# Performance work log

Measured on AMD Instinct MI355X. Metric: run time of the kernel, lower is better.

## Reference

```python
import jax, jax.numpy as jnp
import numpy as np


def _apply_rope(x, cos, sin):
    # x: (b, h, L, D); cos/sin: (b, 1, L, D//2)
    b, h, L, D = x.shape
    xr = x.reshape(b, h, L, D // 2, 2)
    xre, xim = xr[..., 0], xr[..., 1]
    out_re = xre * cos - xim * sin
    out_im = xre * sin + xim * cos
    return jnp.stack([out_re, out_im], axis=-1).reshape(b, h, L, D)


def setup_inputs() -> dict:
    key = jax.random.key(0)
    k1, k2, k3, k4 = jax.random.split(key, 4)
    B, H, L, D = 1, 24, 4096, 128
    q = jax.random.normal(k1, (B, H, L, D), dtype=jnp.float32)
    k = jax.random.normal(k2, (B, H, L, D), dtype=jnp.float32)
    v = jax.random.normal(k3, (B, H, L, D), dtype=jnp.float32)
    positional_encoding = jax.random.normal(k4, (B, L, D // 2, 2), dtype=jnp.float32)
    return {"q": q, "k": k, "v": v, "positional_encoding": positional_encoding}


def reference(q, k, v, positional_encoding):
    # freqs_cis expanded over head axis: (b, 1, L, D//2)
    cos = positional_encoding[:, None, :, :, 0]
    sin = positional_encoding[:, None, :, :, 1]
    qr = _apply_rope(q, cos, sin)
    kr = _apply_rope(k, cos, sin)
    D = q.shape[-1]
    scale = 1.0 / jnp.sqrt(jnp.asarray(D, dtype=q.dtype))
    # (b, h, L, S)
    attn = jnp.einsum("bhld,bhsd->bhls", qr, kr) * scale
    attn = jax.nn.softmax(attn, axis=-1)
    x = jnp.einsum("bhls,bhsd->bhld", attn, v)
    # (b, L, h, d) -> (b, L, h*d)
    b, h, L, d = x.shape
    return jnp.transpose(x, (0, 2, 1, 3)).reshape(b, L, h * d)
```

## Files before the change

kernel.cpp:

```cpp
#include <hip/hip_runtime.h>
#include <hip/hip_bf16.h>

#define H 24
#define L 4096
#define Dh 128
#define QBLK 128
#define KVBLK 64
#define NQT (L/QBLK)
#define NKT (L/KVBLK)

typedef __bf16 bf16;
typedef bf16 bf16x8 __attribute__((ext_vector_type(8)));
typedef bf16 bf16x4 __attribute__((ext_vector_type(4)));
typedef bf16 bf16x2 __attribute__((ext_vector_type(2)));
typedef float f32x4 __attribute__((ext_vector_type(4)));
typedef float f32x16 __attribute__((ext_vector_type(16)));
typedef unsigned u32x4 __attribute__((ext_vector_type(4)));

__device__ __forceinline__ void rope4(const float4& x, const float4& cs, float* o) {
  o[0] = x.x*cs.x - x.y*cs.y;
  o[1] = x.x*cs.y + x.y*cs.x;
  o[2] = x.z*cs.z - x.w*cs.w;
  o[3] = x.z*cs.w + x.w*cs.z;
}

__device__ __forceinline__ unsigned cvt_pk_bf16(float lo, float hi_) {
  unsigned r;
  asm("v_cvt_pk_bf16_f32 %0, %1, %2" : "=v"(r) : "v"(lo), "v"(hi_));
  return r;
}

__device__ __forceinline__ void pl_swap(unsigned &a, unsigned &b) {
#if __has_builtin(__builtin_amdgcn_permlane32_swap)
  typedef unsigned u32x2_t __attribute__((ext_vector_type(2)));
  u32x2_t r = __builtin_amdgcn_permlane32_swap(a, b, false, false);
  a = r.x; b = r.y;
#else
  asm("v_permlane32_swap_b32 %0, %1" : "+v"(a), "+v"(b));
#endif
}

template<int BASE>
__device__ __forceinline__ bf16x8 pack_frag(const f32x16& s) {
  unsigned a0 = cvt_pk_bf16(s[BASE+0], s[BASE+1]);
  unsigned a1 = cvt_pk_bf16(s[BASE+2], s[BASE+3]);
  unsigned b0 = cvt_pk_bf16(s[BASE+4], s[BASE+5]);
  unsigned b1 = cvt_pk_bf16(s[BASE+6], s[BASE+7]);
  pl_swap(a0, b0);
  pl_swap(a1, b1);
  u32x4 v; v[0] = a0; v[1] = a1; v[2] = b0; v[3] = b1;
  return __builtin_bit_cast(bf16x8, v);
}

__device__ __forceinline__ f32x16 zero16() {
  f32x16 v;
#pragma unroll
  for (int i = 0; i < 16; i++) v[i] = 0.f;
  return v;
}

__device__ __forceinline__ void gl16(const void* g, void* l) {
  __builtin_amdgcn_global_load_lds(
      (const __attribute__((address_space(1))) void*)g,
      (__attribute__((address_space(3))) void*)l, 16, 0, 0);
}

__global__ __launch_bounds__(256) void kprep(const float* __restrict__ k,
    const float* __restrict__ pe, bf16* __restrict__ wk) {
  int b = blockIdx.x;
  int h = b >> 7;
  int t = threadIdx.x;
  int l = t & 63, wq = t >> 6, hi = l >> 5;
  int row = (b & 127) * 32 + (l & 31);
  const float* kr = k + ((size_t)h * L + row) * Dh;
  const float* pr = pe + (size_t)row * Dh;
#pragma unroll
  for (int i = 0; i < 2; i++) {
    int ks = wq * 2 + i;
    int d = ks * 16 + hi * 8;
    float4 a  = *(const float4*)(kr + d);
    float4 c  = *(const float4*)(pr + d);
    float4 a2 = *(const float4*)(kr + d + 4);
    float4 c2 = *(const float4*)(pr + d + 4);
    float o[8]; rope4(a, c, o); rope4(a2, c2, o + 4);
    bf16x8 r;
#pragma unroll
    for (int j = 0; j < 8; j++) r[j] = (bf16)o[j];
    *(bf16x8*)(wk + ((size_t)b * 8 + ks) * 512 + l * 8) = r;
  }
}

__global__ __launch_bounds__(256) void vprep(const float* __restrict__ v,
    bf16* __restrict__ wv) {
  __shared__ bf16 T[64][132];
  int b = blockIdx.x;
  int h = b >> 6, G = b & 63;
  int t = threadIdx.x;
  {
    int row = t >> 2, c0 = (t & 3) * 32;
    const float* src = v + ((size_t)h * L + G * 64 + row) * Dh + c0;
#pragma unroll
    for (int i = 0; i < 8; i++) {
      float4 a = ((const float4*)src)[i];
      T[row][c0 + i*4 + 0] = (bf16)a.x; T[row][c0 + i*4 + 1] = (bf16)a.y;
      T[row][c0 + i*4 + 2] = (bf16)a.z; T[row][c0 + i*4 + 3] = (bf16)a.w;
    }
  }
  __syncthreads();
  int l = t & 63, wq = t >> 6, hi = l >> 5, l31 = l & 31;
#pragma unroll
  for (int dt = 0; dt < 4; dt++) {
    bf16x8 r;
#pragma unroll
    for (int j = 0; j < 8; j++) r[j] = T[wq * 16 + hi * 8 + j][dt * 32 + l31];
    *(bf16x8*)(wv + (((size_t)h * 256 + G * 4 + wq) * 4 + dt) * 512 + l * 8) = r;
  }
}

__device__ __forceinline__ void attn5_iter(
    const char* kb, char* kn, int t,
    const char* kg0, const bf16* vgl, int wo, int lane, int hi,
    const bf16x8 (&qf)[8], f32x16 (&acc)[4], float& m, float& lsum) {
  asm volatile("s_waitcnt vmcnt(0)" ::: "memory");
  __builtin_amdgcn_s_barrier();
  __builtin_amdgcn_sched_barrier(0);
  if (t + 1 < NKT) {
    const char* ks_ = kg0 + (size_t)(t + 1) * 16384;
    gl16(ks_,        kn + wo);
    gl16(ks_ + 1024, kn + wo + 1024);
    gl16(ks_ + 2048, kn + wo + 2048);
    gl16(ks_ + 3072, kn + wo + 3072);
  }
  __builtin_amdgcn_sched_barrier(0);

  f32x16 s0 = zero16(), s1 = zero16();
  __builtin_amdgcn_s_setprio(1);
#pragma unroll
  for (int ks = 0; ks < 8; ks++) {
    bf16x8 k0 = *(const bf16x8*)(kb + ks * 1024 + lane * 16);
    s0 = __builtin_amdgcn_mfma_f32_32x32x16_bf16(k0, qf[ks], s0, 0, 0, 0);
    bf16x8 k1 = *(const bf16x8*)(kb + 8192 + ks * 1024 + lane * 16);
    s1 = __builtin_amdgcn_mfma_f32_32x32x16_bf16(k1, qf[ks], s1, 0, 0, 0);
  }
  __builtin_amdgcn_s_setprio(0);

  float t8[8];
#pragma unroll
  for (int i = 0; i < 8; i++)
    t8[i] = fmaxf(fmaxf(s0[i], s0[i + 8]), fmaxf(s1[i], s1[i + 8]));
#pragma unroll
  for (int i = 0; i < 4; i++) t8[i] = fmaxf(t8[i], t8[i + 4]);
  float tm = fmaxf(fmaxf(t8[0], t8[1]), fmaxf(t8[2], t8[3]));
  tm = fmaxf(tm, __shfl_xor(tm, 32, 64));
  if (__any(tm > m + 8.f)) {
    float mn = fmaxf(m, tm);
    float alpha = __builtin_amdgcn_exp2f(m - mn);
    m = mn;
    lsum *= alpha;
#pragma unroll
    for (int r = 0; r < 16; r++) {
      int cr = (r & 3) + 8 * (r >> 2) + 4 * hi;
      float ar = __shfl(alpha, cr, 64);
#pragma unroll
      for (int dt = 0; dt < 4; dt++) acc[dt][r] *= ar;
    }
  }
#pragma unroll
  for (int r = 0; r < 16; r++) {
    s0[r] = __builtin_amdgcn_exp2f(s0[r] - m);
    s1[r] = __builtin_amdgcn_exp2f(s1[r] - m);
  }
  {
    float s8[8];
#pragma unroll
    for (int i = 0; i < 8; i++) s8[i] = (s0[i] + s0[i + 8]) + (s1[i] + s1[i + 8]);
#pragma unroll
    for (int i = 0; i < 4; i++) s8[i] += s8[i + 4];
    float rs = (s8[0] + s8[1]) + (s8[2] + s8[3]);
    rs += __shfl_xor(rs, 32, 64);
    lsum += rs;
  }

  bf16x8 pa00 = pack_frag<0>(s0);
  bf16x8 pa01 = pack_frag<8>(s0);
  bf16x8 pa10 = pack_frag<0>(s1);
  bf16x8 pa11 = pack_frag<8>(s1);

  const bf16* vt = vgl + (size_t)t * 8192;
  __builtin_amdgcn_s_setprio(1);
#pragma unroll
  for (int dt = 0; dt < 4; dt++) {
    bf16x8 v0 = *(const bf16x8*)(vt + (0 * 4 + dt) * 512);
    acc[dt] = __builtin_amdgcn_mfma_f32_32x32x16_bf16(pa00, v0, acc[dt], 0, 0, 0);
    bf16x8 v1 = *(const bf16x8*)(vt + (1 * 4 + dt) * 512);
    acc[dt] = __builtin_amdgcn_mfma_f32_32x32x16_bf16(pa01, v1, acc[dt], 0, 0, 0);
    bf16x8 v2 = *(const bf16x8*)(vt + (2 * 4 + dt) * 512);
    acc[dt] = __builtin_amdgcn_mfma_f32_32x32x16_bf16(pa10, v2, acc[dt], 0, 0, 0);
    bf16x8 v3 = *(const bf16x8*)(vt + (3 * 4 + dt) * 512);
    acc[dt] = __builtin_amdgcn_mfma_f32_32x32x16_bf16(pa11, v3, acc[dt], 0, 0, 0);
  }
  __builtin_amdgcn_s_setprio(0);
}

__global__ __launch_bounds__(256, 3) void attn5(
    const float* __restrict__ q, const float* __restrict__ pe,
    const bf16* __restrict__ wk, const bf16* __restrict__ wv,
    float* __restrict__ out) {
  __shared__ __align__(16) char Kb0[16384], Kb1[16384];

  int bid = (int)blockIdx.x;
  int swz = (bid & 7) * (H * NQT / 8) + (bid >> 3);
  int h = swz >> 5, qt = swz & 31;
  int tid = threadIdx.x;
  int w = tid >> 6, lane = tid & 63;
  int l31 = lane & 31, hi = lane >> 5;
  int wo = w * 4096;

  const float SC = 0.08838834764831845f * 1.4426950408889634f;

  int qrow = qt * QBLK + w * 32 + l31;
  bf16x8 qf[8];
  {
    const float* qp = q + ((size_t)h * L + qrow) * Dh;
    const float* pp = pe + (size_t)qrow * Dh;
#pragma unroll
    for (int ks = 0; ks < 8; ks++) {
      int d = ks * 16 + hi * 8;
      float4 a  = *(const float4*)(qp + d);
      float4 c  = *(const float4*)(pp + d);
      float4 a2 = *(const float4*)(qp + d + 4);
      float4 c2 = *(const float4*)(pp + d + 4);
      float o[8]; rope4(a, c, o); rope4(a2, c2, o + 4);
#pragma unroll
      for (int j = 0; j < 8; j++) qf[ks][j] = (bf16)(o[j] * SC);
    }
  }

  f32x16 acc[4];
#pragma unroll
  for (int dt = 0; dt < 4; dt++) acc[dt] = zero16();
  float m = -3.0e38f, lsum = 0.f;

  const char* kg0 = (const char*)(wk + (size_t)h * 524288) + wo + lane * 16;
  const bf16* vgl = wv + (size_t)h * 524288 + lane * 8;

  gl16(kg0,        Kb0 + wo);
  gl16(kg0 + 1024, Kb0 + wo + 1024);
  gl16(kg0 + 2048, Kb0 + wo + 2048);
  gl16(kg0 + 3072, Kb0 + wo + 3072);

#pragma unroll 1
  for (int tt = 0; tt < NKT / 2; ++tt) {
    attn5_iter(Kb0, Kb1, 2 * tt,     kg0, vgl, wo, lane, hi, qf, acc, m, lsum);
    attn5_iter(Kb1, Kb0, 2 * tt + 1, kg0, vgl, wo, lane, hi, qf, acc, m, lsum);
  }

#pragma unroll
  for (int r = 0; r < 16; r++) {
    int cr = (r & 3) + 8 * (r >> 2) + 4 * hi;
    float ls = __shfl(lsum, cr, 64);
    float inv = 1.0f / ls;
    size_t orow = (size_t)(qt * QBLK + w * 32 + cr);
    float* op = out + orow * (H * Dh) + h * Dh + l31;
#pragma unroll
    for (int dt = 0; dt < 4; dt++) op[dt * 32] = acc[dt][r] * inv;
  }
}

__global__ __launch_bounds__(512) void attn_fb(
    const float* __restrict__ q, const float* __restrict__ kg,
    const float* __restrict__ vg, const float* __restrict__ pe,
    float* __restrict__ out) {
  __shared__ __align__(16) char KsB[KVBLK * Dh * 2];
  __shared__ __align__(16) char VtB[Dh * (KVBLK + 8) * 2];
  __shared__ __align__(16) bf16 Ps[8][16 * KVBLK];

  int bid = (int)blockIdx.x;
  int swz = (bid & 7) * (NQT * H / 8) + (bid >> 3);
  int h  = swz >> 5;
  int qt = swz & 31;
  int tid = threadIdx.x;
  int w = tid >> 6, lane = tid & 63;
  int l16 = lane & 15, lg = lane >> 4;

  const float SC = 0.08838834764831845f * 1.4426950408889634f;

  int qr = qt * QBLK + w * 16 + l16;
  bf16x8 qf[4];
  {
    const float* qrow  = q  + ((size_t)h * L + qr) * Dh;
    const float* perow = pe + (size_t)qr * Dh;
#pragma unroll
    for (int kk = 0; kk < 4; kk++) {
      int d = kk * 32 + lg * 8;
      float4 a  = *(const float4*)(qrow + d);
      float4 b  = *(const float4*)(qrow + d + 4);
      float4 ca = *(const float4*)(perow + d);
      float4 cb = *(const float4*)(perow + d + 4);
      float o[8]; rope4(a, ca, o); rope4(b, cb, o + 4);
#pragma unroll
      for (int j = 0; j < 8; j++) qf[kk][j] = (bf16)(o[j] * SC);
    }
  }

  float m[4], lsum[4];
  f32x4 acc[8];
#pragma unroll
  for (int r = 0; r < 4; r++) { m[r] = -3.0e38f; lsum[r] = 0.f; }
#pragma unroll
  for (int j = 0; j < 8; j++) acc[j] = (f32x4){0.f, 0.f, 0.f, 0.f};

  int krow_s = tid >> 3;
  int kd_s   = (tid & 7) * 16;
  int vd_s   = (tid & 31) * 4;
  int vp_s   = tid >> 5;
  char* psb = (char*)&Ps[w][0];

  for (int t = 0; t < NKT; t++) {
    int kv0 = t * KVBLK;
    {
      bf16 ko[16];
      const float* src = kg + ((size_t)h * L + kv0 + krow_s) * Dh + kd_s;
      const float* ps  = pe + (size_t)(kv0 + krow_s) * Dh + kd_s;
#pragma unroll
      for (int c = 0; c < 4; c++) {
        float4 a  = *(const float4*)(src + c * 4);
        float4 cs = *(const float4*)(ps + c * 4);
        float o[4]; rope4(a, cs, o);
        ko[c*4+0]=(bf16)o[0]; ko[c*4+1]=(bf16)o[1];
        ko[c*4+2]=(bf16)o[2]; ko[c*4+3]=(bf16)o[3];
      }
#pragma unroll
      for (int c = 0; c < 2; c++) {
        int byte = (krow_s * 256 + (kd_s + c * 8) * 2) ^ ((krow_s & 7) << 4);
        *(bf16x8*)(KsB + byte) = *(bf16x8*)(ko + c * 8);
      }
    }
#pragma unroll
    for (int pi = 0; pi < 2; pi++) {
      int p = vp_s + pi * 16;
      int r0 = 2 * p;
      float4 fa = *(const float4*)(vg + ((size_t)h * L + kv0 + r0)     * Dh + vd_s);
      float4 fb = *(const float4*)(vg + ((size_t)h * L + kv0 + r0 + 1) * Dh + vd_s);
      bf16x4 a4, b4;
      a4[0]=(bf16)fa.x; a4[1]=(bf16)fa.y; a4[2]=(bf16)fa.z; a4[3]=(bf16)fa.w;
      b4[0]=(bf16)fb.x; b4[1]=(bf16)fb.y; b4[2]=(bf16)fb.z; b4[3]=(bf16)fb.w;
#pragma unroll
      for (int j = 0; j < 4; j++) {
        bf16x2 pr; pr[0] = a4[j]; pr[1] = b4[j];
        *(bf16x2*)(VtB + (vd_s + j) * 144 + r0 * 2) = pr;
      }
    }
    __syncthreads();

    f32x4 s[4];
#pragma unroll
    for (int jt = 0; jt < 4; jt++) {
      f32x4 a_s = (f32x4){0.f, 0.f, 0.f, 0.f};
      int krow = jt * 16 + l16;
#pragma unroll
      for (int kk = 0; kk < 4; kk++) {
        int byte = (krow * 256 + kk * 64 + lg * 16) ^ ((krow & 7) << 4);
        bf16x8 kf = *(const bf16x8*)(KsB + byte);
        a_s = __builtin_amdgcn_mfma_f32_16x16x32_bf16(qf[kk], kf, a_s, 0, 0, 0);
      }
      s[jt] = a_s;
    }

#pragma unroll
    for (int r = 0; r < 4; r++) {
      float tm = fmaxf(fmaxf(s[0][r], s[1][r]), fmaxf(s[2][r], s[3][r]));
#pragma unroll
      for (int off = 1; off < 16; off <<= 1) tm = fmaxf(tm, __shfl_xor(tm, off, 64));
      float mn = fmaxf(m[r], tm);
      float alpha = exp2f(m[r] - mn);
      m[r] = mn;
      float rs = 0.f;
#pragma unroll
      for (int jt = 0; jt < 4; jt++) {
        float pv_ = exp2f(s[jt][r] - mn);
        s[jt][r] = pv_;
        rs += pv_;
      }
#pragma unroll
      for (int off = 1; off < 16; off <<= 1) rs += __shfl_xor(rs, off, 64);
      lsum[r] = lsum[r] * alpha + rs;
#pragma unroll
      for (int j = 0; j < 8; j++) acc[j][r] *= alpha;
    }

#pragma unroll
    for (int jt = 0; jt < 4; jt++)
#pragma unroll
      for (int r = 0; r < 4; r++) {
        int row = lg * 4 + r;
        int byte = (row * 128 + (jt * 16 + l16) * 2) ^ ((row & 7) << 4);
        *(bf16*)(psb + byte) = (bf16)s[jt][r];
      }
    asm volatile("s_waitcnt lgkmcnt(0)" ::: "memory");
    int pb0 = (l16 * 128 + lg * 16) ^ ((l16 & 7) << 4);
    int pb1 = (l16 * 128 + 64 + lg * 16) ^ ((l16 & 7) << 4);
    bf16x8 pf0 = *(const bf16x8*)(psb + pb0);
    bf16x8 pf1 = *(const bf16x8*)(psb + pb1);

#pragma unroll
    for (int jt = 0; jt < 8; jt++) {
      bf16x8 vf0 = *(const bf16x8*)(VtB + (jt * 16 + l16) * 144 + (lg * 8) * 2);
      acc[jt] = __builtin_amdgcn_mfma_f32_16x16x32_bf16(pf0, vf0, acc[jt], 0, 0, 0);
      bf16x8 vf1 = *(const bf16x8*)(VtB + (jt * 16 + l16) * 144 + (32 + lg * 8) * 2);
      acc[jt] = __builtin_amdgcn_mfma_f32_16x16x32_bf16(pf1, vf1, acc[jt], 0, 0, 0);
    }
    __syncthreads();
  }

  float linv[4];
#pragma unroll
  for (int r = 0; r < 4; r++) linv[r] = 1.0f / lsum[r];
  int orow_base = qt * QBLK + w * 16 + lg * 4;
#pragma unroll
  for (int jt = 0; jt < 8; jt++) {
    int col = h * Dh + jt * 16 + l16;
#pragma unroll
    for (int r = 0; r < 4; r++) {
      out[(size_t)(orow_base + r) * (H * Dh) + col] = acc[jt][r] * linv[r];
    }
  }
}

extern "C" void kernel_launch(void* const* d_in, const int* in_sizes, int n_in,
                              void* d_out, int out_size, void* d_ws, size_t ws_size,
                              hipStream_t stream) {
  const float* q  = (const float*)d_in[0];
  const float* k  = (const float*)d_in[1];
  const float* v  = (const float*)d_in[2];
  const float* pe = (const float*)d_in[3];
  float* out = (float*)d_out;
  const size_t elems = (size_t)H * L * Dh;
  const size_t need  = 2 * elems * sizeof(unsigned short);
  if (ws_size >= need) {
    bf16* wk = (bf16*)d_ws;
    bf16* wv = wk + elems;
    kprep<<<H * 128, 256, 0, stream>>>(k, pe, wk);
    vprep<<<H * 64, 256, 0, stream>>>(v, wv);
    attn5<<<H * NQT, 256, 0, stream>>>(q, pe, wk, wv, out);
  } else {
    attn_fb<<<H * NQT, 512, 0, stream>>>(q, k, v, pe, out);
  }
}
```

Measured before the change: 276.5 us.

## Read K fragments directly from global memory instead of LDS double buffer

Removes the LDS double-buffered K staging (global_load_lds plus per-iteration waitcnt and barrier) and has each wave load its prearranged K fragments straight from global memory, as V already is. This drops the block-wide barrier and the shared-memory footprint, which may allow more independent wave progress. The cost is that the four waves of a block no longer share one K tile load, so they rely on L1/L2 for reuse, and global latency is now exposed directly in the QK^T MFMA loop with no explicit prefetch.

Result: slower. 442.7 us (+60.1%).

```diff
diff --git a/kernel.cpp b/kernel.cpp
--- a/kernel.cpp
+++ b/kernel.cpp
@@ -59,12 +59,6 @@
   return v;
 }
 
-__device__ __forceinline__ void gl16(const void* g, void* l) {
-  __builtin_amdgcn_global_load_lds(
-      (const __attribute__((address_space(1))) void*)g,
-      (__attribute__((address_space(3))) void*)l, 16, 0, 0);
-}
-
 __global__ __launch_bounds__(256) void kprep(const float* __restrict__ k,
     const float* __restrict__ pe, bf16* __restrict__ wk) {
   int b = blockIdx.x;
@@ -117,104 +111,16 @@
   }
 }
 
-__device__ __forceinline__ void attn5_iter(
-    const char* kb, char* kn, int t,
-    const char* kg0, const bf16* vgl, int wo, int lane, int hi,
-    const bf16x8 (&qf)[8], f32x16 (&acc)[4], float& m, float& lsum) {
-  asm volatile("s_waitcnt vmcnt(0)" ::: "memory");
-  __builtin_amdgcn_s_barrier();
-  __builtin_amdgcn_sched_barrier(0);
-  if (t + 1 < NKT) {
-    const char* ks_ = kg0 + (size_t)(t + 1) * 16384;
-    gl16(ks_,        kn + wo);
-    gl16(ks_ + 1024, kn + wo + 1024);
-    gl16(ks_ + 2048, kn + wo + 2048);
-    gl16(ks_ + 3072, kn + wo + 3072);
-  }
-  __builtin_amdgcn_sched_barrier(0);
-
-  f32x16 s0 = zero16(), s1 = zero16();
-  __builtin_amdgcn_s_setprio(1);
-#pragma unroll
-  for (int ks = 0; ks < 8; ks++) {
-    bf16x8 k0 = *(const bf16x8*)(kb + ks * 1024 + lane * 16);
-    s0 = __builtin_amdgcn_mfma_f32_32x32x16_bf16(k0, qf[ks], s0, 0, 0, 0);
-    bf16x8 k1 = *(const bf16x8*)(kb + 8192 + ks * 1024 + lane * 16);
-    s1 = __builtin_amdgcn_mfma_f32_32x32x16_bf16(k1, qf[ks], s1, 0, 0, 0);
-  }
-  __builtin_amdgcn_s_setprio(0);
-
-  float t8[8];
-#pragma unroll
-  for (int i = 0; i < 8; i++)
-    t8[i] = fmaxf(fmaxf(s0[i], s0[i + 8]), fmaxf(s1[i], s1[i + 8]));
-#pragma unroll
-  for (int i = 0; i < 4; i++) t8[i] = fmaxf(t8[i], t8[i + 4]);
-  float tm = fmaxf(fmaxf(t8[0], t8[1]), fmaxf(t8[2], t8[3]));
-  tm = fmaxf(tm, __shfl_xor(tm, 32, 64));
-  if (__any(tm > m + 8.f)) {
-    float mn = fmaxf(m, tm);
-    float alpha = __builtin_amdgcn_exp2f(m - mn);
-    m = mn;
-    lsum *= alpha;
-#pragma unroll
-    for (int r = 0; r < 16; r++) {
-      int cr = (r & 3) + 8 * (r >> 2) + 4 * hi;
-      float ar = __shfl(alpha, cr, 64);
-#pragma unroll
-      for (int dt = 0; dt < 4; dt++) acc[dt][r] *= ar;
-    }
-  }
-#pragma unroll
-  for (int r = 0; r < 16; r++) {
-    s0[r] = __builtin_amdgcn_exp2f(s0[r] - m);
-    s1[r] = __builtin_amdgcn_exp2f(s1[r] - m);
-  }
-  {
-    float s8[8];
-#pragma unroll
-    for (int i = 0; i < 8; i++) s8[i] = (s0[i] + s0[i + 8]) + (s1[i] + s1[i + 8]);
-#pragma unroll
-    for (int i = 0; i < 4; i++) s8[i] += s8[i + 4];
-    float rs = (s8[0] + s8[1]) + (s8[2] + s8[3]);
-    rs += __shfl_xor(rs, 32, 64);
-    lsum += rs;
-  }
-
-  bf16x8 pa00 = pack_frag<0>(s0);
-  bf16x8 pa01 = pack_frag<8>(s0);
-  bf16x8 pa10 = pack_frag<0>(s1);
-  bf16x8 pa11 = pack_frag<8>(s1);
-
-  const bf16* vt = vgl + (size_t)t * 8192;
-  __builtin_amdgcn_s_setprio(1);
-#pragma unroll
-  for (int dt = 0; dt < 4; dt++) {
-    bf16x8 v0 = *(const bf16x8*)(vt + (0 * 4 + dt) * 512);
-    acc[dt] = __builtin_amdgcn_mfma_f32_32x32x16_bf16(pa00, v0, acc[dt], 0, 0, 0);
-    bf16x8 v1 = *(const bf16x8*)(vt + (1 * 4 + dt) * 512);
-    acc[dt] = __builtin_amdgcn_mfma_f32_32x32x16_bf16(pa01, v1, acc[dt], 0, 0, 0);
-    bf16x8 v2 = *(const bf16x8*)(vt + (2 * 4 + dt) * 512);
-    acc[dt] = __builtin_amdgcn_mfma_f32_32x32x16_bf16(pa10, v2, acc[dt], 0, 0, 0);
-    bf16x8 v3 = *(const bf16x8*)(vt + (3 * 4 + dt) * 512);
-    acc[dt] = __builtin_amdgcn_mfma_f32_32x32x16_bf16(pa11, v3, acc[dt], 0, 0, 0);
-  }
-  __builtin_amdgcn_s_setprio(0);
-}
-
-__global__ __launch_bounds__(256, 3) void attn5(
+__global__ __launch_bounds__(256, 3) void attn8(
     const float* __restrict__ q, const float* __restrict__ pe,
     const bf16* __restrict__ wk, const bf16* __restrict__ wv,
     float* __restrict__ out) {
-  __shared__ __align__(16) char Kb0[16384], Kb1[16384];
-
   int bid = (int)blockIdx.x;
   int swz = (bid & 7) * (H * NQT / 8) + (bid >> 3);
   int h = swz >> 5, qt = swz & 31;
   int tid = threadIdx.x;
   int w = tid >> 6, lane = tid & 63;
   int l31 = lane & 31, hi = lane >> 5;
-  int wo = w * 4096;
 
   const float SC = 0.08838834764831845f * 1.4426950408889634f;
 
@@ -241,18 +147,80 @@
   for (int dt = 0; dt < 4; dt++) acc[dt] = zero16();
   float m = -3.0e38f, lsum = 0.f;
 
-  const char* kg0 = (const char*)(wk + (size_t)h * 524288) + wo + lane * 16;
+  const bf16* kgl = wk + (size_t)h * 524288 + lane * 8;
   const bf16* vgl = wv + (size_t)h * 524288 + lane * 8;
 
-  gl16(kg0,        Kb0 + wo);
-  gl16(kg0 + 1024, Kb0 + wo + 1024);
-  gl16(kg0 + 2048, Kb0 + wo + 2048);
-  gl16(kg0 + 3072, Kb0 + wo + 3072);
-
-#pragma unroll 1
-  for (int tt = 0; tt < NKT / 2; ++tt) {
-    attn5_iter(Kb0, Kb1, 2 * tt,     kg0, vgl, wo, lane, hi, qf, acc, m, lsum);
-    attn5_iter(Kb1, Kb0, 2 * tt + 1, kg0, vgl, wo, lane, hi, qf, acc, m, lsum);
+#pragma unroll 2
+  for (int t = 0; t < NKT; ++t) {
+    const bf16* kt = kgl + (size_t)t * 8192;
+
+    f32x16 s0 = zero16(), s1 = zero16();
+    __builtin_amdgcn_s_setprio(1);
+#pragma unroll
+    for (int ks = 0; ks < 8; ks++) {
+      bf16x8 k0 = *(const bf16x8*)(kt + ks * 512);
+      s0 = __builtin_amdgcn_mfma_f32_32x32x16_bf16(k0, qf[ks], s0, 0, 0, 0);
+      bf16x8 k1 = *(const bf16x8*)(kt + 4096 + ks * 512);
+      s1 = __builtin_amdgcn_mfma_f32_32x32x16_bf16(k1, qf[ks], s1, 0, 0, 0);
+    }
+    __builtin_amdgcn_s_setprio(0);
+
+    float t8[8];
+#pragma unroll
+    for (int i = 0; i < 8; i++)
+      t8[i] = fmaxf(fmaxf(s0[i], s0[i + 8]), fmaxf(s1[i], s1[i + 8]));
+#pragma unroll
+    for (int i = 0; i < 4; i++) t8[i] = fmaxf(t8[i], t8[i + 4]);
+    float tm = fmaxf(fmaxf(t8[0], t8[1]), fmaxf(t8[2], t8[3]));
+    tm = fmaxf(tm, __shfl_xor(tm, 32, 64));
+    if (__any(tm > m + 8.f)) {
+      float mn = fmaxf(m, tm);
+      float alpha = __builtin_amdgcn_exp2f(m - mn);
+      m = mn;
+      lsum *= alpha;
+#pragma unroll
+      for (int r = 0; r < 16; r++) {
+        int cr = (r & 3) + 8 * (r >> 2) + 4 * hi;
+        float ar = __shfl(alpha, cr, 64);
+#pragma unroll
+        for (int dt = 0; dt < 4; dt++) acc[dt][r] *= ar;
+      }
+    }
+#pragma unroll
+    for (int r = 0; r < 16; r++) {
+      s0[r] = __builtin_amdgcn_exp2f(s0[r] - m);
+      s1[r] = __builtin_amdgcn_exp2f(s1[r] - m);
+    }
+    {
+      float s8[8];
+#pragma unroll
+      for (int i = 0; i < 8; i++) s8[i] = (s0[i] + s0[i + 8]) + (s1[i] + s1[i + 8]);
+#pragma unroll
+      for (int i = 0; i < 4; i++) s8[i] += s8[i + 4];
+      float rs = (s8[0] + s8[1]) + (s8[2] + s8[3]);
+      rs += __shfl_xor(rs, 32, 64);
+      lsum += rs;
+    }
+
+    bf16x8 pa00 = pack_frag<0>(s0);
+    bf16x8 pa01 = pack_frag<8>(s0);
+    bf16x8 pa10 = pack_frag<0>(s1);
+    bf16x8 pa11 = pack_frag<8>(s1);
+
+    const bf16* vt = vgl + (size_t)t * 8192;
+    __builtin_amdgcn_s_setprio(1);
+#pragma unroll
+    for (int dt = 0; dt < 4; dt++) {
+      bf16x8 v0 = *(const bf16x8*)(vt + (0 * 4 + dt) * 512);
+      acc[dt] = __builtin_amdgcn_mfma_f32_32x32x16_bf16(pa00, v0, acc[dt], 0, 0, 0);
+      bf16x8 v1 = *(const bf16x8*)(vt + (1 * 4 + dt) * 512);
+      acc[dt] = __builtin_amdgcn_mfma_f32_32x32x16_bf16(pa01, v1, acc[dt], 0, 0, 0);
+      bf16x8 v2 = *(const bf16x8*)(vt + (2 * 4 + dt) * 512);
+      acc[dt] = __builtin_amdgcn_mfma_f32_32x32x16_bf16(pa10, v2, acc[dt], 0, 0, 0);
+      bf16x8 v3 = *(const bf16x8*)(vt + (3 * 4 + dt) * 512);
+      acc[dt] = __builtin_amdgcn_mfma_f32_32x32x16_bf16(pa11, v3, acc[dt], 0, 0, 0);
+    }
+    __builtin_amdgcn_s_setprio(0);
   }
 
 #pragma unroll
@@ -442,7 +410,7 @@
     bf16* wv = wk + elems;
     kprep<<<H * 128, 256, 0, stream>>>(k, pe, wk);
     vprep<<<H * 64, 256, 0, stream>>>(v, wv);
-    attn5<<<H * NQT, 256, 0, stream>>>(q, pe, wk, wv, out);
+    attn8<<<H * NQT, 256, 0, stream>>>(q, pe, wk, wv, out);
   } else {
     attn_fb<<<H * NQT, 512, 0, stream>>>(q, k, v, pe, out);
   }
```

## Stage V tiles through shared memory via async global-to-LDS loads

Applied to the files above, without the earlier changes.

V fragments were previously read directly from global memory in the PV MFMA loop. Now each iteration issues async global-to-LDS loads of the current V tile into a new 16KB shared buffer alongside the next K prefetch, then waits for the V portion with a partial vmcnt and a barrier before the PV MFMAs. The goal is to hide V load latency and turn scattered per-lane global reads into LDS reads. In exchange it adds an extra barrier per iteration, raises LDS use to 48KB per block, and always issues a wrapped-around K prefetch on the last iteration. Because V is not double-buffered, its load is only overlapped with the QK and softmax work.

Measured after the change: 251.4 us. -9.1%, faster.

```diff
diff --git a/kernel.cpp b/kernel.cpp
--- a/kernel.cpp
+++ b/kernel.cpp
@@ -117,15 +117,23 @@
   }
 }
 
-__device__ __forceinline__ void attn5_iter(
-    const char* kb, char* kn, int t,
-    const char* kg0, const bf16* vgl, int wo, int lane, int hi,
+__device__ __forceinline__ void attn9_iter(
+    const char* kb, char* kn, char* vb, int t,
+    const char* kg0, const char* vg0, int wo, int lane, int hi,
     const bf16x8 (&qf)[8], f32x16 (&acc)[4], float& m, float& lsum) {
   asm volatile("s_waitcnt vmcnt(0)" ::: "memory");
   __builtin_amdgcn_s_barrier();
   __builtin_amdgcn_sched_barrier(0);
-  if (t + 1 < NKT) {
-    const char* ks_ = kg0 + (size_t)(t + 1) * 16384;
+  {
+    const char* vs_ = vg0 + (size_t)t * 16384;
+    gl16(vs_,        vb + wo);
+    gl16(vs_ + 1024, vb + wo + 1024);
+    gl16(vs_ + 2048, vb + wo + 2048);
+    gl16(vs_ + 3072, vb + wo + 3072);
+  }
+  {
+    int tn = (t + 1) & (NKT - 1);
+    const char* ks_ = kg0 + (size_t)tn * 16384;
     gl16(ks_,        kn + wo);
     gl16(ks_ + 1024, kn + wo + 1024);
     gl16(ks_ + 2048, kn + wo + 2048);
@@ -186,27 +194,31 @@
   bf16x8 pa10 = pack_frag<0>(s1);
   bf16x8 pa11 = pack_frag<8>(s1);
 
-  const bf16* vt = vgl + (size_t)t * 8192;
+  asm volatile("s_waitcnt vmcnt(4)" ::: "memory");
+  __builtin_amdgcn_s_barrier();
+  __builtin_amdgcn_sched_barrier(0);
+
   __builtin_amdgcn_s_setprio(1);
 #pragma unroll
   for (int dt = 0; dt < 4; dt++) {
-    bf16x8 v0 = *(const bf16x8*)(vt + (0 * 4 + dt) * 512);
+    bf16x8 v0 = *(const bf16x8*)(vb + (0 * 4 + dt) * 1024 + lane * 16);
     acc[dt] = __builtin_amdgcn_mfma_f32_32x32x16_bf16(pa00, v0, acc[dt], 0, 0, 0);
-    bf16x8 v1 = *(const bf16x8*)(vt + (1 * 4 + dt) * 512);
+    bf16x8 v1 = *(const bf16x8*)(vb + (1 * 4 + dt) * 1024 + lane * 16);
     acc[dt] = __builtin_amdgcn_mfma_f32_32x32x16_bf16(pa01, v1, acc[dt], 0, 0, 0);
-    bf16x8 v2 = *(const bf16x8*)(vt + (2 * 4 + dt) * 512);
+    bf16x8 v2 = *(const bf16x8*)(vb + (2 * 4 + dt) * 1024 + lane * 16);
     acc[dt] = __builtin_amdgcn_mfma_f32_32x32x16_bf16(pa10, v2, acc[dt], 0, 0, 0);
-    bf16x8 v3 = *(const bf16x8*)(vt + (3 * 4 + dt) * 512);
+    bf16x8 v3 = *(const bf16x8*)(vb + (3 * 4 + dt) * 1024 + lane * 16);
     acc[dt] = __builtin_amdgcn_mfma_f32_32x32x16_bf16(pa11, v3, acc[dt], 0, 0, 0);
   }
   __builtin_amdgcn_s_setprio(0);
 }
 
-__global__ __launch_bounds__(256, 3) void attn5(
+__global__ __launch_bounds__(256, 3) void attn9(
     const float* __restrict__ q, const float* __restrict__ pe,
     const bf16* __restrict__ wk, const bf16* __restrict__ wv,
     float* __restrict__ out) {
   __shared__ __align__(16) char Kb0[16384], Kb1[16384];
+  __shared__ __align__(16) char Vb[16384];
 
   int bid = (int)blockIdx.x;
   int swz = (bid & 7) * (H * NQT / 8) + (bid >> 3);
@@ -242,7 +254,7 @@
   float m = -3.0e38f, lsum = 0.f;
 
   const char* kg0 = (const char*)(wk + (size_t)h * 524288) + wo + lane * 16;
-  const bf16* vgl = wv + (size_t)h * 524288 + lane * 8;
+  const char* vg0 = (const char*)(wv + (size_t)h * 524288) + wo + lane * 16;
 
   gl16(kg0,        Kb0 + wo);
   gl16(kg0 + 1024, Kb0 + wo + 1024);
@@ -251,9 +263,10 @@
 
 #pragma unroll 1
   for (int tt = 0; tt < NKT / 2; ++tt) {
-    attn5_iter(Kb0, Kb1, 2 * tt,     kg0, vgl, wo, lane, hi, qf, acc, m, lsum);
-    attn5_iter(Kb1, Kb0, 2 * tt + 1, kg0, vgl, wo, lane, hi, qf, acc, m, lsum);
-  }
+    attn9_iter(Kb0, Kb1, Vb, 2 * tt,     kg0, vg0, wo, lane, hi, qf, acc, m, lsum);
+    attn9_iter(Kb1, Kb0, Vb, 2 * tt + 1, kg0, vg0, wo, lane, hi, qf, acc, m, lsum);
+  }
+  asm volatile("s_waitcnt vmcnt(0)" ::: "memory");
 
 #pragma unroll
   for (int r = 0; r < 16; r++) {
@@ -442,7 +455,7 @@
     bf16* wv = wk + elems;
     kprep<<<H * 128, 256, 0, stream>>>(k, pe, wk);
     vprep<<<H * 64, 256, 0, stream>>>(v, wv);
-    attn5<<<H * NQT, 256, 0, stream>>>(q, pe, wk, wv, out);
+    attn9<<<H * NQT, 256, 0, stream>>>(q, pe, wk, wv, out);
   } else {
     attn_fb<<<H * NQT, 512, 0, stream>>>(q, k, v, pe, out);
   }
```
